# Kernel optimization log

Hardware: AMD Instinct MI355X
Metric: run time of the kernel (lower is better)

## Reference

```python
import jax, jax.numpy as jnp
import numpy as np

V, ENC, D, E = 10000, 2048, 512, 512
B, L = 128, 64


def setup_inputs() -> dict:
    key = jax.random.key(0)
    ks = jax.random.split(key, 12)
    s = lambda *sh: 1.0 / np.sqrt(sh[-1])
    return {
        "global_feats": jax.random.normal(ks[0], (B, ENC), jnp.float32),
        "encoded_captions": jax.random.randint(ks[1], (B, L), 0, V, jnp.int64),
        "caption_lengths": jax.random.randint(ks[2], (B,), 1, L, jnp.int64),
        "W_embed": jax.random.normal(ks[3], (V, E), jnp.float32) * 0.02,
        "W_init": jax.random.normal(ks[4], (D, ENC), jnp.float32) * s(ENC),
        "b_init": jnp.zeros((D,), jnp.float32),
        "W_ih": jax.random.normal(ks[5], (3 * D, E), jnp.float32) * s(E),
        "W_hh": jax.random.normal(ks[6], (3 * D, D), jnp.float32) * s(D),
        "b_ih": jnp.zeros((3 * D,), jnp.float32),
        "b_hh": jnp.zeros((3 * D,), jnp.float32),
        "W_fc": jax.random.normal(ks[7], (V, D), jnp.float32) * s(D),
        "b_fc": jnp.zeros((V,), jnp.float32),
    }


def reference(global_feats, encoded_captions, caption_lengths,
              W_embed, W_init, b_init, W_ih, W_hh, b_ih, b_hh, W_fc, b_fc):
    # init_hidden: h0 = tanh(Linear(global_feats))  -> (B, D)
    h0 = jnp.tanh(global_feats @ W_init.T + b_init)

    # teacher forcing over timesteps 0..L-2 (PyTorch GRU gate order: r, z, n)
    emb = W_embed[encoded_captions[:, : L - 1]]          # (B, L-1, E)
    gi = jnp.einsum('ble,ge->blg', emb, W_ih) + b_ih     # (B, L-1, 3D) precomputed input gates
    gi = jnp.swapaxes(gi, 0, 1)                          # (L-1, B, 3D) scan over time

    def step(h, gi_t):
        gh = h @ W_hh.T + b_hh                           # (B, 3D)
        i_r, i_z, i_n = jnp.split(gi_t, 3, axis=-1)
        h_r, h_z, h_n = jnp.split(gh, 3, axis=-1)
        r = jax.nn.sigmoid(i_r + h_r)
        z = jax.nn.sigmoid(i_z + h_z)
        n = jnp.tanh(i_n + r * h_n)
        h_new = (1.0 - z) * n + z * h
        return h_new, h_new

    _, hs = jax.lax.scan(step, h0, gi)                   # hs: (L-1, B, D)
    # dropout is identity in eval/reference mode
    logits = jnp.einsum('lbd,vd->blv', hs, W_fc) + b_fc  # (B, L-1, V)
    return logits, caption_lengths - 1
```

## Files before the change

### kernel.cpp

```cpp
#include <hip/hip_runtime.h>
#include <hip/hip_bf16.h>

#define V_    10000
#define ENC_  2048
#define D_    512
#define B_    128
#define L_    64
#define T_    63
#define M_    (B_ * L_ - B_)
#define G_    (3 * D_)
#define LOGITS_SZ ((long)M_ * V_)
#define SCAN_NB 64

typedef __bf16 bf16x8_t __attribute__((ext_vector_type(8)));
typedef float  f32x4_t  __attribute__((ext_vector_type(4)));
typedef short  s16x8_t  __attribute__((ext_vector_type(8)));

typedef __attribute__((address_space(3))) char*       lds_cptr_t;
typedef const __attribute__((address_space(1))) char* glb_cptr_t;

__device__ __forceinline__ void gload_lds16(const void* g, void* l) {
  __builtin_amdgcn_global_load_lds((glb_cptr_t)g, (lds_cptr_t)l, 16, 0, 0);
}
__device__ __forceinline__ float bf2f(short s) {
  return __uint_as_float(((unsigned)(unsigned short)s) << 16);
}
__device__ __forceinline__ short f2bf(float f) {
  __hip_bfloat16 h = __float2bfloat16(f);
  return *reinterpret_cast<short*>(&h);
}
__device__ __forceinline__ s16x8_t cvt8(const float* p) {
  f32x4_t lo = *reinterpret_cast<const f32x4_t*>(p);
  f32x4_t hi = *reinterpret_cast<const f32x4_t*>(p + 4);
  s16x8_t r;
#pragma unroll
  for (int e = 0; e < 4; e++) { r[e] = f2bf(lo[e]); r[4 + e] = f2bf(hi[e]); }
  return r;
}
__device__ __forceinline__ float sigmoidf_(float x) {
  return 1.0f / (1.0f + __expf(-x));
}
__device__ __forceinline__ bf16x8_t lds_frag(const short* p) {
  return __builtin_bit_cast(bf16x8_t, *reinterpret_cast<const s16x8_t*>(p));
}

__global__ void GG_cvt5(const float* __restrict__ whh, __hip_bfloat16* __restrict__ dwhh,
                        const float* __restrict__ wih, __hip_bfloat16* __restrict__ dwih,
                        const float* __restrict__ wemb, __hip_bfloat16* __restrict__ dwemb,
                        const float* __restrict__ winit, __hip_bfloat16* __restrict__ dwinit,
                        const float* __restrict__ gf, __hip_bfloat16* __restrict__ dgf) {
  const int i = blockIdx.x * blockDim.x + threadIdx.x;
  const float* s; __hip_bfloat16* d; int off;
  if (i < 98304)        { s = whh;   d = dwhh;   off = i; }
  else if (i < 196608)  { s = wih;   d = dwih;   off = i - 98304; }
  else if (i < 836608)  { s = wemb;  d = dwemb;  off = i - 196608; }
  else if (i < 967680)  { s = winit; d = dwinit; off = i - 836608; }
  else                  { s = gf;    d = dgf;    off = i - 967680; }
  s16x8_t v = cvt8(s + (long)off * 8);
  *reinterpret_cast<s16x8_t*>(d + (long)off * 8) = v;
}

__global__ void GG_cvt_kernel(const float* __restrict__ src,
                              __hip_bfloat16* __restrict__ dst, int n8) {
  int i = blockIdx.x * blockDim.x + threadIdx.x;
  if (i < n8) {
    s16x8_t v = cvt8(src + (long)i * 8);
    *reinterpret_cast<s16x8_t*>(dst + (long)i * 8) = v;
  }
}

__global__ __launch_bounds__(256) void GG_gemm_h0(
    const __hip_bfloat16* __restrict__ gfB,
    const __hip_bfloat16* __restrict__ WinitB,
    const float* __restrict__ binit,
    __hip_bfloat16* __restrict__ hfull) {
  __shared__ short sA[128 * 64];
  __shared__ short sB[128 * 64];
  const int lane = threadIdx.x & 63;
  const int wave = threadIdx.x >> 6;
  const int n0 = blockIdx.x * 128;
  const int srow = lane >> 3;
  const int scol = (lane & 7) * 8;

  f32x4_t acc[4][4] = {};

  const __hip_bfloat16* aptr[4];
  const __hip_bfloat16* bptr[4];
#pragma unroll
  for (int i = 0; i < 4; i++) {
    const int r = (wave * 4 + i) * 8 + srow;
    aptr[i] = gfB + (long)r * ENC_ + scol;
    bptr[i] = WinitB + (long)(n0 + r) * ENC_ + scol;
  }

  const int wm = (wave >> 1) * 64;
  const int wn = (wave & 1) * 64;
  const int fr = lane & 15;
  const int fk = (lane >> 4) * 8;

  for (int kt = 0; kt < 32; kt++) {
    __syncthreads();
#pragma unroll
    for (int i = 0; i < 4; i++) {
      const int chunk = wave * 4 + i;
      gload_lds16(aptr[i] + kt * 64, sA + chunk * 512);
      gload_lds16(bptr[i] + kt * 64, sB + chunk * 512);
    }
    __syncthreads();
#pragma unroll
    for (int kk = 0; kk < 2; kk++) {
      bf16x8_t a[4], b[4];
#pragma unroll
      for (int i = 0; i < 4; i++) {
        a[i] = lds_frag(sA + (wm + i * 16 + fr) * 64 + kk * 32 + fk);
        b[i] = lds_frag(sB + (wn + i * 16 + fr) * 64 + kk * 32 + fk);
      }
#pragma unroll
      for (int i = 0; i < 4; i++)
#pragma unroll
        for (int j = 0; j < 4; j++)
          acc[i][j] = __builtin_amdgcn_mfma_f32_16x16x32_bf16(a[i], b[j], acc[i][j], 0, 0, 0);
    }
  }

  const int fq = lane >> 4;
#pragma unroll
  for (int j = 0; j < 4; j++) {
    const int n = n0 + wn + j * 16 + fr;
    const float bv = binit[n];
#pragma unroll
    for (int i = 0; i < 4; i++)
#pragma unroll
      for (int rr = 0; rr < 4; rr++) {
        const int m = wm + i * 16 + fq * 4 + rr;
        hfull[(long)m * 64 * 512 + n] = __float2bfloat16(tanhf(acc[i][j][rr] + bv));
      }
  }
}

__global__ __launch_bounds__(256) void GG_gemm_gi(
    const __hip_bfloat16* __restrict__ WembB,
    const int* __restrict__ cap,
    const __hip_bfloat16* __restrict__ WihB,
    const float* __restrict__ bias,
    __hip_bfloat16* __restrict__ C) {
  __shared__ short sA[128 * 64];
  __shared__ short sB[128 * 64];
  const int lane = threadIdx.x & 63;
  const int wave = threadIdx.x >> 6;
  const int m0 = blockIdx.y * 128;
  const int n0 = blockIdx.x * 128;
  const int srow = lane >> 3;
  const int scol = (lane & 7) * 8;

  f32x4_t acc[4][4] = {};

  const __hip_bfloat16* aptr[4];
  const __hip_bfloat16* bptr[4];
#pragma unroll
  for (int i = 0; i < 4; i++) {
    const int r = (wave * 4 + i) * 8 + srow;
    const int bt = m0 + r;
    const int bb = bt / 63;
    const int tt = bt - bb * 63;
    aptr[i] = WembB + (long)cap[bb * L_ + tt] * 512 + scol;
    bptr[i] = WihB + (long)(n0 + r) * 512 + scol;
  }

  const int wm = (wave >> 1) * 64;
  const int wn = (wave & 1) * 64;
  const int fr = lane & 15;
  const int fk = (lane >> 4) * 8;

  for (int kt = 0; kt < 8; kt++) {
    __syncthreads();
#pragma unroll
    for (int i = 0; i < 4; i++) {
      const int chunk = wave * 4 + i;
      gload_lds16(aptr[i] + kt * 64, sA + chunk * 512);
      gload_lds16(bptr[i] + kt * 64, sB + chunk * 512);
    }
    __syncthreads();
#pragma unroll
    for (int kk = 0; kk < 2; kk++) {
      bf16x8_t a[4], b[4];
#pragma unroll
      for (int i = 0; i < 4; i++) {
        a[i] = lds_frag(sA + (wm + i * 16 + fr) * 64 + kk * 32 + fk);
        b[i] = lds_frag(sB + (wn + i * 16 + fr) * 64 + kk * 32 + fk);
      }
#pragma unroll
      for (int i = 0; i < 4; i++)
#pragma unroll
        for (int j = 0; j < 4; j++)
          acc[i][j] = __builtin_amdgcn_mfma_f32_16x16x32_bf16(a[i], b[j], acc[i][j], 0, 0, 0);
    }
  }

  const int fq = lane >> 4;
#pragma unroll
  for (int j = 0; j < 4; j++) {
    const int n = n0 + wn + j * 16 + fr;
    const float bv = bias[n];
#pragma unroll
    for (int i = 0; i < 4; i++)
#pragma unroll
      for (int rr = 0; rr < 4; rr++) {
        const int m = m0 + wm + i * 16 + fq * 4 + rr;
        C[(long)m * G_ + n] = __float2bfloat16(acc[i][j][rr] + bv);
      }
  }
}

template <bool BBF16>
__global__ __launch_bounds__(256) void GG_gemm_logits(
    const __hip_bfloat16* __restrict__ hfull,
    const void* __restrict__ Bsrc,
    const float* __restrict__ bias,
    float* __restrict__ C) {
  const int flat = blockIdx.x;
  const int xcd = flat & 7;
  const int s = flat >> 3;
  const int col = xcd * 10 + s % 10;
  const int row = s / 10;
  if (col >= 79) return;
  const int m0 = row * 128;
  const int n0 = col * 128;

  __shared__ short sA[128 * 64];
  __shared__ short sB[128 * 64];
  const int lane = threadIdx.x & 63;
  const int wave = threadIdx.x >> 6;
  const int srow = lane >> 3;
  const int scol = (lane & 7) * 8;

  f32x4_t acc[4][4] = {};

  const __hip_bfloat16* aptr[4];
  const __hip_bfloat16* bptrB[4];
  const float* bptrF[4];
#pragma unroll
  for (int i = 0; i < 4; i++) {
    const int r = (wave * 4 + i) * 8 + srow;
    const int m = m0 + r;
    const int bb = m / 63;
    const int tt = m - bb * 63;
    aptr[i] = hfull + ((long)bb * 64 + tt + 1) * 512 + scol;
    int nrow = n0 + r;
    nrow = (nrow < V_) ? nrow : (V_ - 1);
    if constexpr (BBF16) bptrB[i] = (const __hip_bfloat16*)Bsrc + (long)nrow * 512 + scol;
    else                 bptrF[i] = (const float*)Bsrc + (long)nrow * 512 + scol;
  }

  const int wm = (wave >> 1) * 64;
  const int wn = (wave & 1) * 64;
  const int fr = lane & 15;
  const int fk = (lane >> 4) * 8;

  for (int kt = 0; kt < 8; kt++) {
    s16x8_t vb[4];
    if constexpr (!BBF16) {
#pragma unroll
      for (int i = 0; i < 4; i++) vb[i] = cvt8(bptrF[i] + kt * 64);
    }
    __syncthreads();
#pragma unroll
    for (int i = 0; i < 4; i++) {
      const int chunk = wave * 4 + i;
      gload_lds16(aptr[i] + kt * 64, sA + chunk * 512);
      if constexpr (BBF16)
        gload_lds16(bptrB[i] + kt * 64, sB + chunk * 512);
      else
        *reinterpret_cast<s16x8_t*>(sB + chunk * 512 + lane * 8) = vb[i];
    }
    __syncthreads();
#pragma unroll
    for (int kk = 0; kk < 2; kk++) {
      bf16x8_t a[4], b[4];
#pragma unroll
      for (int i = 0; i < 4; i++) {
        a[i] = lds_frag(sA + (wm + i * 16 + fr) * 64 + kk * 32 + fk);
        b[i] = lds_frag(sB + (wn + i * 16 + fr) * 64 + kk * 32 + fk);
      }
#pragma unroll
      for (int i = 0; i < 4; i++)
#pragma unroll
        for (int j = 0; j < 4; j++)
          acc[i][j] = __builtin_amdgcn_mfma_f32_16x16x32_bf16(a[i], b[j], acc[i][j], 0, 0, 0);
    }
  }

  const int fq = lane >> 4;
#pragma unroll
  for (int j = 0; j < 4; j++) {
    const int n = n0 + wn + j * 16 + fr;
    if (n >= V_) continue;
    const float bv = bias[n];
#pragma unroll
    for (int i = 0; i < 4; i++)
#pragma unroll
      for (int rr = 0; rr < 4; rr++) {
        const int m = m0 + wm + i * 16 + fq * 4 + rr;
        C[(long)m * V_ + n] = acc[i][j][rr] + bv;
      }
  }
}

__global__ __launch_bounds__(256) void GG_scan_persist(
    __hip_bfloat16* __restrict__ hfull,
    const __hip_bfloat16* __restrict__ gi,
    const __hip_bfloat16* __restrict__ WhhB,
    const float* __restrict__ bhh,
    int* __restrict__ flagbase) {
  __shared__ short sW[48 * 512];
  const int lane = threadIdx.x & 63;
  const int wave = threadIdx.x >> 6;
  const int strip = blockIdx.x & 31;
  const int half  = blockIdx.x >> 5;
  const int d0 = strip * 16;
  const int fr = lane & 15;
  const int g4 = lane >> 4;
  int* myflags = flagbase + half * 32;

  for (int rr = wave; rr < 48; rr += 4) {
    const int grow = (rr >> 4) * 512 + d0 + (rr & 15);
    gload_lds16(WhhB + (long)grow * 512 + (lane ^ (rr & 7)) * 8, sW + rr * 512);
  }

  const int dd = d0 + fr;
  const int bbase = half * 64 + wave * 16 + g4 * 4;
  const float br_ = bhh[dd], bz_ = bhh[512 + dd], bn_ = bhh[1024 + dd];
  const short* gis = (const short*)gi;

  const int arow = half * 64 + wave * 16 + fr;
  const unsigned long long abase0 =
      (unsigned long long)hfull + ((unsigned long long)arow * 64 * 512 + (unsigned)(g4 * 8)) * 2ull;

  unsigned long long sbase[4];
#pragma unroll
  for (int rr = 0; rr < 4; rr++)
    sbase[rr] = (unsigned long long)hfull +
                ((unsigned long long)(bbase + rr) * 64 * 512 + (unsigned)dd) * 2ull;

  float hp[4];
#pragma unroll
  for (int rr = 0; rr < 4; rr++)
    hp[rr] = bf2f(*(const short*)&hfull[((long)(bbase + rr) * 64) * 512 + dd]);

  asm volatile("s_waitcnt vmcnt(0)" ::: "memory");
  __syncthreads();

  for (int t = 0; t < T_; t++) {
    short gir[4], giz[4], gin[4];
#pragma unroll
    for (int rr = 0; rr < 4; rr++) {
      const long gbase = ((long)(bbase + rr) * T_ + t) * (long)G_;
      gir[rr] = gis[gbase + dd];
      giz[rr] = gis[gbase + 512 + dd];
      gin[rr] = gis[gbase + 1024 + dd];
    }

    if (t > 0) {
      if (threadIdx.x < 64) {
        while (true) {
          int v = t;
          if (lane < 32)
            v = __hip_atomic_load(&myflags[lane], __ATOMIC_RELAXED,
                                  __HIP_MEMORY_SCOPE_SYSTEM);
          if (__all(v >= t)) break;
          __builtin_amdgcn_s_sleep(1);
        }
      }
      __syncthreads();
    }

    const unsigned long long ab = abase0 + (unsigned long long)t * 1024ull;
    f32x4_t a[16];
#define ALOAD(IDX, OFF)                                                        \
    asm volatile("global_load_dwordx4 %0, %1, off offset:" #OFF " sc0 sc1"     \
                 : "=v"(a[IDX]) : "v"(ab));
    ALOAD(0, 0)    ALOAD(1, 64)   ALOAD(2, 128)  ALOAD(3, 192)
    ALOAD(4, 256)  ALOAD(5, 320)  ALOAD(6, 384)  ALOAD(7, 448)
    ALOAD(8, 512)  ALOAD(9, 576)  ALOAD(10, 640) ALOAD(11, 704)
    ALOAD(12, 768) ALOAD(13, 832) ALOAD(14, 896) ALOAD(15, 960)
#undef ALOAD
    asm volatile("s_waitcnt vmcnt(0)" ::: "memory");
    __builtin_amdgcn_sched_barrier(0);

    f32x4_t acc[3] = {};
#pragma unroll
    for (int kt = 0; kt < 16; kt++) {
      const bf16x8_t afr = __builtin_bit_cast(bf16x8_t, a[kt]);
      const int gsw = ((kt * 4 + g4) ^ (fr & 7)) * 8;
      bf16x8_t bfr[3];
#pragma unroll
      for (int j = 0; j < 3; j++) bfr[j] = lds_frag(sW + (j * 16 + fr) * 512 + gsw);
#pragma unroll
      for (int j = 0; j < 3; j++)
        acc[j] = __builtin_amdgcn_mfma_f32_16x16x32_bf16(afr, bfr[j], acc[j], 0, 0, 0);
    }

#pragma unroll
    for (int rr = 0; rr < 4; rr++) {
      const float rg = sigmoidf_(bf2f(gir[rr]) + acc[0][rr] + br_);
      const float zg = sigmoidf_(bf2f(giz[rr]) + acc[1][rr] + bz_);
      const float ng = tanhf(bf2f(gin[rr]) + rg * (acc[2][rr] + bn_));
      const short hnb = f2bf((1.f - zg) * ng + zg * hp[rr]);
      hp[rr] = bf2f(hnb);
      const unsigned long long saddr = sbase[rr] + (unsigned long long)(t + 1) * 1024ull;
      const unsigned int val = (unsigned short)hnb;
      asm volatile("global_store_short %0, %1, off sc0 sc1"
                   :: "v"(saddr), "v"(val) : "memory");
    }

    if (t < T_ - 1) {
      asm volatile("s_waitcnt vmcnt(0)" ::: "memory");
      __syncthreads();
      if (threadIdx.x == 0)
        __hip_atomic_store(&myflags[strip], t + 1, __ATOMIC_RELAXED,
                           __HIP_MEMORY_SCOPE_SYSTEM);
    }
  }
}

__global__ void GG_tail_kernel(const int* __restrict__ lens, float* __restrict__ out) {
  const int b = threadIdx.x;
  if (b < B_) out[LOGITS_SZ + b] = (float)(lens[b] - 1);
}

extern "C" void kernel_launch(void* const* d_in, const int* in_sizes, int n_in,
                              void* d_out, int out_size, void* d_ws, size_t ws_size,
                              hipStream_t stream) {
  const float* gf      = (const float*)d_in[0];
  const int*   cap     = (const int*)d_in[1];
  const int*   lens    = (const int*)d_in[2];
  const float* W_embed = (const float*)d_in[3];
  const float* W_init  = (const float*)d_in[4];
  const float* b_init  = (const float*)d_in[5];
  const float* W_ih    = (const float*)d_in[6];
  const float* W_hh    = (const float*)d_in[7];
  const float* b_ih    = (const float*)d_in[8];
  const float* b_hh    = (const float*)d_in[9];
  const float* W_fc    = (const float*)d_in[10];
  const float* b_fc    = (const float*)d_in[11];
  float* out = (float*)d_out;

  char* ob = (char*)d_out;
  __hip_bfloat16* gi_ws  = (__hip_bfloat16*)ob;
  __hip_bfloat16* WhhB   = (__hip_bfloat16*)(ob + 25165824);
  __hip_bfloat16* WihB   = (__hip_bfloat16*)(ob + 27262976);
  __hip_bfloat16* WembB  = (__hip_bfloat16*)(ob + 29360128);
  __hip_bfloat16* WinitB = (__hip_bfloat16*)(ob + 40894464);
  __hip_bfloat16* gfB    = (__hip_bfloat16*)(ob + 43253760);

  __hip_bfloat16* hfull = (__hip_bfloat16*)d_ws;
  __hip_bfloat16* WfcB  = (__hip_bfloat16*)((char*)d_ws + 8388608);
  const bool big_ws = ws_size >= (size_t)(8388608 + 10240000 + 256);
  int* flags = (int*)((char*)d_ws + (big_ws ? 18628608 : 8388608));

  hipMemsetAsync(flags, 0, 256, stream);

  GG_cvt5<<<dim3(3908), 256, 0, stream>>>(W_hh, WhhB, W_ih, WihB, W_embed, WembB,
                                          W_init, WinitB, gf, gfB);
  if (big_ws)
    GG_cvt_kernel<<<dim3((V_ * D_ / 8 + 255) / 256), 256, 0, stream>>>(W_fc, WfcB, V_ * D_ / 8);

  GG_gemm_h0<<<dim3(4), 256, 0, stream>>>(gfB, WinitB, b_init, hfull);

  GG_gemm_gi<<<dim3(G_ / 128, M_ / 128), 256, 0, stream>>>(WembB, cap, WihB, b_ih, gi_ws);

  GG_scan_persist<<<dim3(SCAN_NB), 256, 0, stream>>>(hfull, gi_ws, WhhB, b_hh, flags);

  if (big_ws)
    GG_gemm_logits<true><<<dim3(5040), 256, 0, stream>>>(hfull, WfcB, b_fc, out);
  else
    GG_gemm_logits<false><<<dim3(5040), 256, 0, stream>>>(hfull, W_fc, b_fc, out);

  GG_tail_kernel<<<dim3(1), 128, 0, stream>>>(lens, out);
}
```

Measured before the change: 587.6 us.

## Prefetch next-step input gates and poll flags in every wave of GRU scan

The recurrent GRU scan kernel now issues the input-gate loads for step t+1 during step t, right after the hidden-state loads, and waits on a partial vmcnt so those loads overlap the MFMA and gate math. The cross-block flag wait is also changed: every wave now spins on the flags itself, replacing the single polling wave followed by a block-wide barrier. Both changes aim to shorten the per-timestep latency chain of the sequential scan. The cost is more atomic polling traffic and extra registers, and the hand-counted vmcnt(12) depends on the exact number of loads in flight.

```diff
diff --git a/kernel.cpp b/kernel.cpp
--- a/kernel.cpp
+++ b/kernel.cpp
@@ -15,6 +15,7 @@
 typedef __bf16 bf16x8_t __attribute__((ext_vector_type(8)));
 typedef float  f32x4_t  __attribute__((ext_vector_type(4)));
 typedef short  s16x8_t  __attribute__((ext_vector_type(8)));
+typedef unsigned long long ull_t;
 
 typedef __attribute__((address_space(3))) char*       lds_cptr_t;
 typedef const __attribute__((address_space(1))) char* glb_cptr_t;
@@ -333,48 +334,42 @@
   const short* gis = (const short*)gi;
 
   const int arow = half * 64 + wave * 16 + fr;
-  const unsigned long long abase0 =
-      (unsigned long long)hfull + ((unsigned long long)arow * 64 * 512 + (unsigned)(g4 * 8)) * 2ull;
-
-  unsigned long long sbase[4];
-#pragma unroll
-  for (int rr = 0; rr < 4; rr++)
-    sbase[rr] = (unsigned long long)hfull +
-                ((unsigned long long)(bbase + rr) * 64 * 512 + (unsigned)dd) * 2ull;
-
+  const ull_t abase0 =
+      (ull_t)hfull + ((ull_t)arow * 64 * 512 + (unsigned)(g4 * 8)) * 2ull;
+
+  ull_t sbase[4];
+  const short* gp0[4];
+#pragma unroll
+  for (int rr = 0; rr < 4; rr++) {
+    sbase[rr] = (ull_t)hfull +
+                ((ull_t)(bbase + rr) * 64 * 512 + (unsigned)dd) * 2ull;
+    gp0[rr] = gis + (long)(bbase + rr) * T_ * G_ + dd;
+  }
+
+  unsigned cr[4], cz[4], cn[4];
   float hp[4];
 #pragma unroll
-  for (int rr = 0; rr < 4; rr++)
+  for (int rr = 0; rr < 4; rr++) {
+    cr[rr] = (unsigned short)gp0[rr][0];
+    cz[rr] = (unsigned short)gp0[rr][512];
+    cn[rr] = (unsigned short)gp0[rr][1024];
     hp[rr] = bf2f(*(const short*)&hfull[((long)(bbase + rr) * 64) * 512 + dd]);
+  }
 
   asm volatile("s_waitcnt vmcnt(0)" ::: "memory");
   __syncthreads();
 
   for (int t = 0; t < T_; t++) {
-    short gir[4], giz[4], gin[4];
-#pragma unroll
-    for (int rr = 0; rr < 4; rr++) {
-      const long gbase = ((long)(bbase + rr) * T_ + t) * (long)G_;
-      gir[rr] = gis[gbase + dd];
-      giz[rr] = gis[gbase + 512 + dd];
-      gin[rr] = gis[gbase + 1024 + dd];
-    }
-
     if (t > 0) {
-      if (threadIdx.x < 64) {
-        while (true) {
-          int v = t;
-          if (lane < 32)
-            v = __hip_atomic_load(&myflags[lane], __ATOMIC_RELAXED,
-                                  __HIP_MEMORY_SCOPE_SYSTEM);
-          if (__all(v >= t)) break;
-          __builtin_amdgcn_s_sleep(1);
-        }
-      }
-      __syncthreads();
-    }
-
-    const unsigned long long ab = abase0 + (unsigned long long)t * 1024ull;
+      while (true) {
+        const int v = __hip_atomic_load(&myflags[lane & 31], __ATOMIC_RELAXED,
+                                        __HIP_MEMORY_SCOPE_SYSTEM);
+        if (__all(v >= t)) break;
+        __builtin_amdgcn_s_sleep(1);
+      }
+    }
+
+    const ull_t ab = abase0 + (ull_t)t * 1024ull;
     f32x4_t a[16];
 #define ALOAD(IDX, OFF)                                                        \
     asm volatile("global_load_dwordx4 %0, %1, off offset:" #OFF " sc0 sc1"     \
@@ -384,7 +379,18 @@
     ALOAD(8, 512)  ALOAD(9, 576)  ALOAD(10, 640) ALOAD(11, 704)
     ALOAD(12, 768) ALOAD(13, 832) ALOAD(14, 896) ALOAD(15, 960)
 #undef ALOAD
-    asm volatile("s_waitcnt vmcnt(0)" ::: "memory");
+
+    const int tp = (t < T_ - 1) ? (t + 1) : (T_ - 1);
+    unsigned nr[4], nz[4], nn[4];
+#pragma unroll
+    for (int rr = 0; rr < 4; rr++) {
+      const short* gp = gp0[rr] + (long)tp * G_;
+      asm volatile("global_load_ushort %0, %1, off"             : "=v"(nr[rr]) : "v"(gp));
+      asm volatile("global_load_ushort %0, %1, off offset:1024" : "=v"(nz[rr]) : "v"(gp));
+      asm volatile("global_load_ushort %0, %1, off offset:2048" : "=v"(nn[rr]) : "v"(gp));
+    }
+
+    asm volatile("s_waitcnt vmcnt(12)" ::: "memory");
     __builtin_amdgcn_sched_barrier(0);
 
     f32x4_t acc[3] = {};
@@ -402,19 +408,23 @@
 
 #pragma unroll
     for (int rr = 0; rr < 4; rr++) {
-      const float rg = sigmoidf_(bf2f(gir[rr]) + acc[0][rr] + br_);
-      const float zg = sigmoidf_(bf2f(giz[rr]) + acc[1][rr] + bz_);
-      const float ng = tanhf(bf2f(gin[rr]) + rg * (acc[2][rr] + bn_));
+      const float rg = sigmoidf_(bf2f((short)cr[rr]) + acc[0][rr] + br_);
+      const float zg = sigmoidf_(bf2f((short)cz[rr]) + acc[1][rr] + bz_);
+      const float ng = tanhf(bf2f((short)cn[rr]) + rg * (acc[2][rr] + bn_));
       const short hnb = f2bf((1.f - zg) * ng + zg * hp[rr]);
       hp[rr] = bf2f(hnb);
-      const unsigned long long saddr = sbase[rr] + (unsigned long long)(t + 1) * 1024ull;
+      const ull_t saddr = sbase[rr] + (ull_t)(t + 1) * 1024ull;
       const unsigned int val = (unsigned short)hnb;
       asm volatile("global_store_short %0, %1, off sc0 sc1"
                    :: "v"(saddr), "v"(val) : "memory");
     }
 
+    asm volatile("s_waitcnt vmcnt(0)" ::: "memory");
+    __builtin_amdgcn_sched_barrier(0);
+#pragma unroll
+    for (int rr = 0; rr < 4; rr++) { cr[rr] = nr[rr]; cz[rr] = nz[rr]; cn[rr] = nn[rr]; }
+
     if (t < T_ - 1) {
-      asm volatile("s_waitcnt vmcnt(0)" ::: "memory");
       __syncthreads();
       if (threadIdx.x == 0)
         __hip_atomic_store(&myflags[strip], t + 1, __ATOMIC_RELAXED,
```

New measurement: 558.3 us. 5.0% less time.
